# Kernel tuning notes

Hardware: AMD Instinct MI355X
Metric: run time of the kernel (lower is better)

The kernel has to match this reference:

```python
import jax, jax.numpy as jnp
import numpy as np
import math

BITS = 4
THRESH = 0.999
N_HEADS = 32
KV_HEADS = 8
HEAD_DIM = 128
ROPE_THETA = 10000.0


def _lower_median(x, axis):
    # torch.median returns the LOWER of the two middle values for even n
    n = x.shape[axis]
    xs = jnp.sort(x, axis=axis)
    return jnp.take(xs, jnp.array([(n - 1) // 2]), axis=axis)  # keepdims


def fake_quant_sparse(x, bits, axis, thresh):
    # simulated_quantize with include_sparse=True, dynamicquantization=True,
    # first_few_fp16=-1, clamp=False (faithful to KVQuant quant_fn_zp)
    x = x.astype(jnp.float32)
    t = 1.0 - (1.0 - thresh) / 2.0
    upper = jnp.quantile(x, t, axis=axis, keepdims=True)
    lower = jnp.quantile(x, 1.0 - t, axis=axis, keepdims=True)
    mask = (x <= lower) | (x >= upper)  # outlier mask
    med = _lower_median(x, axis)
    outliers = x * mask
    tmp = x - outliers + med * mask  # replace outliers with median
    maxval = jnp.max(tmp, axis=axis, keepdims=True)
    minval = jnp.min(tmp, axis=axis, keepdims=True)
    qx = (2 ** bits - 1) / (maxval - minval)
    offset = minval * qx  # clamp=False path
    inp = x - outliers
    q = jnp.clip(jnp.round(qx * inp - offset), 0.0, 2 ** bits - 1)
    deq = (q + offset) / qx
    out = jnp.where(mask, x, deq)  # qinp_out[mask]=0 then + outliers
    return jnp.nan_to_num(out, nan=0.0, posinf=0.0, neginf=0.0)


def _rotate_half(x):
    h = x.shape[-1] // 2
    return jnp.concatenate([-x[..., h:], x[..., :h]], axis=-1)


def _rope_cos_sin(position_ids, head_dim, theta):
    inv_freq = 1.0 / (theta ** (jnp.arange(0, head_dim, 2, dtype=jnp.float32) / head_dim))
    freqs = position_ids.astype(jnp.float32)[..., None] * inv_freq  # [B,S,hd/2]
    emb = jnp.concatenate([freqs, freqs], axis=-1)                   # [B,S,hd]
    return jnp.cos(emb), jnp.sin(emb)


def setup_inputs() -> dict:
    key = jax.random.key(0)
    ks = jax.random.split(key, 5)
    B, S, H = 2, 1024, 4096
    kv_dim = KV_HEADS * HEAD_DIM
    scale = 1.0 / math.sqrt(H)
    hidden_states = jax.random.normal(ks[0], (B, S, H), jnp.float32)
    Wq = jax.random.normal(ks[1], (H, H), jnp.float32) * scale
    Wk = jax.random.normal(ks[2], (kv_dim, H), jnp.float32) * scale
    Wv = jax.random.normal(ks[3], (kv_dim, H), jnp.float32) * scale
    Wo = jax.random.normal(ks[4], (H, H), jnp.float32) * scale
    position_ids = jnp.broadcast_to(jnp.arange(S, dtype=jnp.int32)[None, :], (B, S))
    attention_mask = jnp.broadcast_to(jnp.tril(jnp.ones((S, S), dtype=bool))[None, None], (B, 1, S, S))
    return {"hidden_states": hidden_states, "Wq": Wq, "Wk": Wk, "Wv": Wv,
            "Wo": Wo, "position_ids": position_ids, "attention_mask": attention_mask}


def reference(hidden_states, Wq, Wk, Wv, Wo, position_ids, attention_mask):
    B, S, H = hidden_states.shape
    groups = N_HEADS // KV_HEADS

    q = (hidden_states @ Wq.T).reshape(B, S, N_HEADS, HEAD_DIM).transpose(0, 2, 1, 3)
    k = hidden_states @ Wk.T  # [B,S,kv_dim]
    v = hidden_states @ Wv.T

    # Pre-RoPE quantization: K per-channel (axis 0 over B*S tokens), V per-token
    k_flat = fake_quant_sparse(k.reshape(B * S, -1), BITS, 0, THRESH)
    v_flat = fake_quant_sparse(v.reshape(B * S, -1), BITS, -1, THRESH)
    k = k_flat.reshape(B, S, KV_HEADS, HEAD_DIM).transpose(0, 2, 1, 3)
    v = v_flat.reshape(B, S, KV_HEADS, HEAD_DIM).transpose(0, 2, 1, 3)

    cos, sin = _rope_cos_sin(position_ids, HEAD_DIM, ROPE_THETA)
    cos, sin = cos[:, None], sin[:, None]  # [B,1,S,hd]
    q = q * cos + _rotate_half(q) * sin
    k = k * cos + _rotate_half(k) * sin

    k = jnp.repeat(k, groups, axis=1)  # repeat_kv -> [B,n_heads,S,hd]
    v = jnp.repeat(v, groups, axis=1)

    scores = jnp.einsum('bhqd,bhkd->bhqk', q, k) / math.sqrt(HEAD_DIM)
    scores = jnp.where(attention_mask, scores, jnp.finfo(jnp.float32).min)
    probs = jax.nn.softmax(scores.astype(jnp.float32), axis=-1).astype(q.dtype)
    attn = jnp.einsum('bhqk,bhkd->bhqd', probs, v)
    attn = attn.transpose(0, 2, 1, 3).reshape(B, S, -1)
    return attn @ Wo.T
```

## Files before the change

kernel.cpp:

```cpp
#include <hip/hip_runtime.h>

#define S_LEN 1024
#define B_SZ 2
#define H_DIM 4096
#define NHEADS 32
#define KVHEADS 8
#define HDIM 128
#define KV_DIM 1024
#define BS_C 2048

typedef _Float16 half8 __attribute__((ext_vector_type(8)));
typedef float f4 __attribute__((ext_vector_type(4)));
typedef unsigned short ushort_t;

static __device__ __forceinline__ ushort_t f2h(float x) {
  _Float16 h = (_Float16)x;
  return __builtin_bit_cast(unsigned short, h);
}
static __device__ __forceinline__ float h2f(ushort_t u) {
  return (float)__builtin_bit_cast(_Float16, u);
}

static __device__ __forceinline__ void gl2lds16(const void* g, void* l) {
  __builtin_amdgcn_global_load_lds(
      (const __attribute__((address_space(1))) unsigned int*)(unsigned long long)(uintptr_t)g,
      (__attribute__((address_space(3))) unsigned int*)(unsigned int)(uintptr_t)l,
      16, 0, 0);
}

__global__ __launch_bounds__(256) void cvt16(const float* __restrict__ x,
                                             ushort_t* __restrict__ h, int n4) {
  int i = blockIdx.x * 256 + threadIdx.x;
  if (i >= n4) return;
  float4 v = ((const float4*)x)[i];
  uint2 hp;
  hp.x = (unsigned)f2h(v.x) | ((unsigned)f2h(v.y) << 16);
  hp.y = (unsigned)f2h(v.z) | ((unsigned)f2h(v.w) << 16);
  ((uint2*)h)[i] = hp;
}

__global__ __launch_bounds__(256) void gemm_qkv(const ushort_t* __restrict__ Ahg,
                                                const ushort_t* __restrict__ Bhg,
                                                ushort_t* __restrict__ Qout,
                                                float* __restrict__ KVout) {
  __shared__ short Ah[128 * 32];
  __shared__ short Bh[128 * 32];
  const int K = 4096;
  const int tid = threadIdx.x;
  const int wid = tid >> 6;
  const int lane = tid & 63;
  const int ln = lane & 15;
  const int quad = lane >> 4;
  const int wx = wid & 1, wy = wid >> 1;
  const int m0 = blockIdx.y * 128, n0 = blockIdx.x * 128;
  const int sr = tid >> 2, sc = (tid & 3) * 8;

  const ushort_t* ap0 = Ahg + (size_t)(m0 + sr) * K + sc;
  const ushort_t* bp0 = Bhg + (size_t)(n0 + sr) * K + sc;
  const size_t rs = (size_t)64 * K;

  f4 acc[4][4];
#pragma unroll
  for (int i = 0; i < 4; i++)
#pragma unroll
    for (int j = 0; j < 4; j++) acc[i][j] = (f4){0.f, 0.f, 0.f, 0.f};

  for (int kk = 0; kk < K; kk += 32) {
    gl2lds16(ap0 + kk,      &Ah[tid * 8]);
    gl2lds16(ap0 + kk + rs, &Ah[2048 + tid * 8]);
    gl2lds16(bp0 + kk,      &Bh[tid * 8]);
    gl2lds16(bp0 + kk + rs, &Bh[2048 + tid * 8]);
    __syncthreads();

    half8 af[4], bfr[4];
#pragma unroll
    for (int mi = 0; mi < 4; mi++)
      af[mi] = *(const half8*)&Ah[(wy * 64 + mi * 16 + ln) * 32 + quad * 8];
#pragma unroll
    for (int ni = 0; ni < 4; ni++)
      bfr[ni] = *(const half8*)&Bh[(wx * 64 + ni * 16 + ln) * 32 + quad * 8];
    __syncthreads();

#pragma unroll
    for (int mi = 0; mi < 4; mi++)
#pragma unroll
      for (int ni = 0; ni < 4; ni++)
        acc[mi][ni] = __builtin_amdgcn_mfma_f32_16x16x32_f16(af[mi], bfr[ni], acc[mi][ni], 0, 0, 0);
  }

#pragma unroll
  for (int mi = 0; mi < 4; mi++) {
    int m = m0 + wy * 64 + mi * 16 + quad * 4;
#pragma unroll
    for (int ni = 0; ni < 4; ni++) {
      int n = n0 + wx * 64 + ni * 16 + ln;
      if (n0 < 4096) {
        ushort_t* cp = Qout + (size_t)m * 4096 + n;
#pragma unroll
        for (int r = 0; r < 4; r++) cp[(size_t)r * 4096] = f2h(acc[mi][ni][r]);
      } else {
        float* cp = KVout + (size_t)m * 2048 + (n - 4096);
#pragma unroll
        for (int r = 0; r < 4; r++) cp[(size_t)r * 2048] = acc[mi][ni][r];
      }
    }
  }
}

__global__ __launch_bounds__(256) void gemm_o(const ushort_t* __restrict__ Ahg,
                                              const ushort_t* __restrict__ Bhg,
                                              float* __restrict__ C0,
                                              float* __restrict__ C1) {
  __shared__ short Ah[128 * 32];
  __shared__ short Bh[128 * 32];
  const int K = 4096;
  const int tid = threadIdx.x;
  const int wid = tid >> 6;
  const int lane = tid & 63;
  const int ln = lane & 15;
  const int quad = lane >> 4;
  const int wx = wid & 1, wy = wid >> 1;
  const int m0 = blockIdx.y * 128, n0 = blockIdx.x * 128;
  const int kz = blockIdx.z * 2048;
  const int sr = tid >> 2, sc = (tid & 3) * 8;

  const ushort_t* ap0 = Ahg + (size_t)(m0 + sr) * K + kz + sc;
  const ushort_t* bp0 = Bhg + (size_t)(n0 + sr) * K + kz + sc;
  const size_t rs = (size_t)64 * K;

  f4 acc[4][4];
#pragma unroll
  for (int i = 0; i < 4; i++)
#pragma unroll
    for (int j = 0; j < 4; j++) acc[i][j] = (f4){0.f, 0.f, 0.f, 0.f};

  for (int kk = 0; kk < 2048; kk += 32) {
    gl2lds16(ap0 + kk,      &Ah[tid * 8]);
    gl2lds16(ap0 + kk + rs, &Ah[2048 + tid * 8]);
    gl2lds16(bp0 + kk,      &Bh[tid * 8]);
    gl2lds16(bp0 + kk + rs, &Bh[2048 + tid * 8]);
    __syncthreads();

    half8 af[4], bfr[4];
#pragma unroll
    for (int mi = 0; mi < 4; mi++)
      af[mi] = *(const half8*)&Ah[(wy * 64 + mi * 16 + ln) * 32 + quad * 8];
#pragma unroll
    for (int ni = 0; ni < 4; ni++)
      bfr[ni] = *(const half8*)&Bh[(wx * 64 + ni * 16 + ln) * 32 + quad * 8];
    __syncthreads();

#pragma unroll
    for (int mi = 0; mi < 4; mi++)
#pragma unroll
      for (int ni = 0; ni < 4; ni++)
        acc[mi][ni] = __builtin_amdgcn_mfma_f32_16x16x32_f16(af[mi], bfr[ni], acc[mi][ni], 0, 0, 0);
  }

  float* Cp = blockIdx.z ? C1 : C0;
#pragma unroll
  for (int mi = 0; mi < 4; mi++) {
    int m = m0 + wy * 64 + mi * 16 + quad * 4;
#pragma unroll
    for (int ni = 0; ni < 4; ni++) {
      int n = n0 + wx * 64 + ni * 16 + ln;
      float* cp = Cp + (size_t)m * 4096 + n;
#pragma unroll
      for (int r = 0; r < 4; r++) cp[(size_t)r * 4096] = acc[mi][ni][r];
    }
  }
}

__global__ __launch_bounds__(256) void reduce2(float* __restrict__ out,
                                               const float* __restrict__ p1, int n4) {
  int i = blockIdx.x * 256 + threadIdx.x;
  if (i >= n4) return;
  float4 a = ((const float4*)out)[i];
  float4 b = ((const float4*)p1)[i];
  a.x += b.x; a.y += b.y; a.z += b.z; a.w += b.w;
  ((float4*)out)[i] = a;
}

__global__ __launch_bounds__(256) void kquant(float* __restrict__ KV) {
  __shared__ float s[2048];
  __shared__ float red[256];
  const int c = blockIdx.x, tid = threadIdx.x;
  float x[8];
#pragma unroll
  for (int i = 0; i < 8; i++) {
    x[i] = KV[(size_t)(tid + i * 256) * 2048 + c];
    s[tid + i * 256] = x[i];
  }
  __syncthreads();
  for (int k = 2; k <= 2048; k <<= 1)
    for (int j = k >> 1; j > 0; j >>= 1) {
      for (int i = tid; i < 2048; i += 256) {
        int l = i ^ j;
        if (l > i) {
          float a = s[i], b2 = s[l];
          bool up = ((i & k) == 0);
          if ((a > b2) == up) { s[i] = b2; s[l] = a; }
        }
      }
      __syncthreads();
    }
  float lower = s[1]    + 0.0235f * (s[2]    - s[1]);
  float upper = s[2045] + 0.9765f * (s[2046] - s[2045]);
  float med   = s[1023];
  float mx = -__builtin_inff(), mn = __builtin_inff();
#pragma unroll
  for (int i = 0; i < 8; i++) {
    bool m = (x[i] <= lower) | (x[i] >= upper);
    float t = m ? med : x[i];
    mx = fmaxf(mx, t);
    mn = fminf(mn, t);
  }
  __syncthreads();
  red[tid] = mx; __syncthreads();
  for (int off = 128; off > 0; off >>= 1) {
    if (tid < off) red[tid] = fmaxf(red[tid], red[tid + off]);
    __syncthreads();
  }
  mx = red[0]; __syncthreads();
  red[tid] = mn; __syncthreads();
  for (int off = 128; off > 0; off >>= 1) {
    if (tid < off) red[tid] = fminf(red[tid], red[tid + off]);
    __syncthreads();
  }
  mn = red[0];
  float qx = 15.0f / (mx - mn);
  float offv = mn * qx;
#pragma unroll
  for (int i = 0; i < 8; i++) {
    bool m = (x[i] <= lower) | (x[i] >= upper);
    float inp = m ? 0.f : x[i];
    float q = rintf(qx * inp - offv);
    q = fminf(fmaxf(q, 0.f), 15.f);
    float deq = (q + offv) / qx;
    float o = m ? x[i] : deq;
    if (!__builtin_isfinite(o)) o = 0.f;
    KV[(size_t)(tid + i * 256) * 2048 + c] = o;
  }
}

__global__ __launch_bounds__(256) void vquant(const float* __restrict__ KV,
                                              ushort_t* __restrict__ vrow) {
  __shared__ float s[1024];
  __shared__ float red[256];
  const int rrow = blockIdx.x, tid = threadIdx.x;
  float x[4];
#pragma unroll
  for (int i = 0; i < 4; i++) {
    x[i] = KV[(size_t)rrow * 2048 + 1024 + tid + i * 256];
    s[tid + i * 256] = x[i];
  }
  __syncthreads();
  for (int k = 2; k <= 1024; k <<= 1)
    for (int j = k >> 1; j > 0; j >>= 1) {
      for (int i = tid; i < 1024; i += 256) {
        int l = i ^ j;
        if (l > i) {
          float a = s[i], b2 = s[l];
          bool up = ((i & k) == 0);
          if ((a > b2) == up) { s[i] = b2; s[l] = a; }
        }
      }
      __syncthreads();
    }
  float lower = s[0]    + 0.5115f * (s[1]    - s[0]);
  float upper = s[1022] + 0.4885f * (s[1023] - s[1022]);
  float med   = s[511];
  float mx = -__builtin_inff(), mn = __builtin_inff();
#pragma unroll
  for (int i = 0; i < 4; i++) {
    bool m = (x[i] <= lower) | (x[i] >= upper);
    float t = m ? med : x[i];
    mx = fmaxf(mx, t);
    mn = fminf(mn, t);
  }
  __syncthreads();
  red[tid] = mx; __syncthreads();
  for (int off = 128; off > 0; off >>= 1) {
    if (tid < off) red[tid] = fmaxf(red[tid], red[tid + off]);
    __syncthreads();
  }
  mx = red[0]; __syncthreads();
  red[tid] = mn; __syncthreads();
  for (int off = 128; off > 0; off >>= 1) {
    if (tid < off) red[tid] = fminf(red[tid], red[tid + off]);
    __syncthreads();
  }
  mn = red[0];
  float qx = 15.0f / (mx - mn);
  float offv = mn * qx;
#pragma unroll
  for (int i = 0; i < 4; i++) {
    bool m = (x[i] <= lower) | (x[i] >= upper);
    float inp = m ? 0.f : x[i];
    float q = rintf(qx * inp - offv);
    q = fminf(fmaxf(q, 0.f), 15.f);
    float deq = (q + offv) / qx;
    float o = m ? x[i] : deq;
    if (!__builtin_isfinite(o)) o = 0.f;
    vrow[(size_t)rrow * 1024 + tid + i * 256] = f2h(o);
  }
}

__global__ __launch_bounds__(256) void vtrans(const ushort_t* __restrict__ vrow,
                                              ushort_t* __restrict__ vb) {
  __shared__ ushort_t T[64 * 65];
  const int c0 = blockIdx.x * 64, r0 = blockIdx.y * 64;
  const int b = r0 >> 10, sbase = r0 & 1023;
#pragma unroll
  for (int i = 0; i < 2; i++) {
    int idx = threadIdx.x + i * 256;
    int r = idx >> 3, c8 = (idx & 7) * 8;
    uint4 v = *(const uint4*)(vrow + (size_t)(r0 + r) * 1024 + c0 + c8);
    const ushort_t* p = (const ushort_t*)&v;
#pragma unroll
    for (int j = 0; j < 8; j++) T[r * 65 + c8 + j] = p[j];
  }
  __syncthreads();
#pragma unroll
  for (int i = 0; i < 2; i++) {
    int idx = threadIdx.x + i * 256;
    int c = idx >> 3, s8 = (idx & 7) * 8;
    ushort_t tmp[8];
#pragma unroll
    for (int j = 0; j < 8; j++) tmp[j] = T[(s8 + j) * 65 + c];
    int gc = c0 + c;
    size_t oa = ((size_t)(b * KVHEADS + (gc >> 7)) * HDIM + (gc & 127)) * S_LEN + sbase + s8;
    *(uint4*)(vb + oa) = *(const uint4*)tmp;
  }
}

__global__ __launch_bounds__(256) void rope_q(const ushort_t* __restrict__ Q,
                                              const int* __restrict__ pos,
                                              ushort_t* __restrict__ qb) {
  int t = blockIdx.x * 256 + threadIdx.x;
  int i = t & 63;
  int h = (t >> 6) & 31;
  int s = (t >> 11) & 1023;
  int b = t >> 21;
  int p = pos[b * S_LEN + s];
  float inv = expf(-9.210340371976184f * ((float)i * (1.0f / 64.0f)));
  float ang = (float)p * inv;
  float sn, cs;
  sincosf(ang, &sn, &cs);
  size_t base = ((size_t)(b * S_LEN + s)) * H_DIM + h * HDIM + i;
  float x1 = h2f(Q[base]), x2 = h2f(Q[base + 64]);
  const float sc = 0.08838834764831845f;
  size_t ob = (((size_t)(b * NHEADS + h)) * S_LEN + s) * HDIM + i;
  qb[ob]      = f2h((x1 * cs - x2 * sn) * sc);
  qb[ob + 64] = f2h((x2 * cs + x1 * sn) * sc);
}

__global__ __launch_bounds__(256) void rope_k(const float* __restrict__ KV,
                                              const int* __restrict__ pos,
                                              ushort_t* __restrict__ kb) {
  int t = blockIdx.x * 256 + threadIdx.x;
  int i = t & 63;
  int h = (t >> 6) & 7;
  int s = (t >> 9) & 1023;
  int b = t >> 19;
  int p = pos[b * S_LEN + s];
  float inv = expf(-9.210340371976184f * ((float)i * (1.0f / 64.0f)));
  float ang = (float)p * inv;
  float sn, cs;
  sincosf(ang, &sn, &cs);
  size_t base = ((size_t)(b * S_LEN + s)) * 2048 + h * HDIM + i;
  float k1 = KV[base], k2 = KV[base + 64];
  size_t ob = (((size_t)(b * KVHEADS + h)) * S_LEN + s) * HDIM + i;
  kb[ob]      = f2h(k1 * cs - k2 * sn);
  kb[ob + 64] = f2h(k2 * cs + k1 * sn);
}

__global__ __launch_bounds__(256) void attn_fwd(const ushort_t* __restrict__ qb,
                                                const ushort_t* __restrict__ kb,
                                                const ushort_t* __restrict__ vb,
                                                ushort_t* __restrict__ ob) {
  __shared__ short Ks[64 * 136];
  __shared__ short Vs[128 * 72];
  __shared__ short Ps[4 * 32 * 72];
  const int tid = threadIdx.x;
  const int wid = tid >> 6;
  const int lane = tid & 63;
  const int ln = lane & 15;
  const int quad = lane >> 4;
  const int q0 = blockIdx.x * 128;
  const int bh = blockIdx.y;
  const int b = bh >> 5, h = bh & 31, hk = h >> 2;

  half8 aq[2][4];
#pragma unroll
  for (int mi = 0; mi < 2; mi++) {
    const ushort_t* qrow =
        qb + (((size_t)(b * NHEADS + h)) * S_LEN + q0 + wid * 32 + mi * 16 + ln) * HDIM;
#pragma unroll
    for (int ks = 0; ks < 4; ks++) aq[mi][ks] = *(const half8*)(qrow + ks * 32 + quad * 8);
  }

  f4 accO[2][8];
#pragma unroll
  for (int mi = 0; mi < 2; mi++)
#pragma unroll
    for (int i = 0; i < 8; i++) accO[mi][i] = (f4){0.f, 0.f, 0.f, 0.f};
  float mr[2][4], lr[2][4];
#pragma unroll
  for (int mi = 0; mi < 2; mi++)
#pragma unroll
    for (int r = 0; r < 4; r++) { mr[mi][r] = -__builtin_inff(); lr[mi][r] = 0.f; }

  const ushort_t* kbp = kb + ((size_t)(b * KVHEADS + hk)) * S_LEN * HDIM;
  const ushort_t* vbp = vb + ((size_t)(b * KVHEADS + hk)) * HDIM * S_LEN;

  const int ktiles = 2 * blockIdx.x + 2;
  for (int kt = 0; kt < ktiles; kt++) {
    const int k0 = kt * 64;
    __syncthreads();
#pragma unroll
    for (int cc = 0; cc < 4; cc++) {
      int idx = tid + cc * 256;
      int r = idx >> 4, c8 = idx & 15;
      *(uint4*)&Ks[r * 136 + c8 * 8] = *(const uint4*)(kbp + (size_t)(k0 + r) * HDIM + c8 * 8);
      int d = idx >> 3, s8 = idx & 7;
      *(uint4*)&Vs[d * 72 + s8 * 8] = *(const uint4*)(vbp + (size_t)d * S_LEN + k0 + s8 * 8);
    }
    __syncthreads();

    if (q0 + wid * 32 + 31 < k0) continue;

    f4 sc[2][4];
#pragma unroll
    for (int mi = 0; mi < 2; mi++)
#pragma unroll
      for (int nt = 0; nt < 4; nt++) sc[mi][nt] = (f4){0.f, 0.f, 0.f, 0.f};
#pragma unroll
    for (int nt = 0; nt < 4; nt++) {
      half8 bk[4];
#pragma unroll
      for (int ks = 0; ks < 4; ks++)
        bk[ks] = *(const half8*)&Ks[(nt * 16 + ln) * 136 + ks * 32 + quad * 8];
#pragma unroll
      for (int mi = 0; mi < 2; mi++)
#pragma unroll
        for (int ks = 0; ks < 4; ks++)
          sc[mi][nt] = __builtin_amdgcn_mfma_f32_16x16x32_f16(aq[mi][ks], bk[ks], sc[mi][nt], 0, 0, 0);
    }
#pragma unroll
    for (int mi = 0; mi < 2; mi++)
#pragma unroll
      for (int r = 0; r < 4; r++) {
        int mq = q0 + wid * 32 + mi * 16 + quad * 4 + r;
#pragma unroll
        for (int nt = 0; nt < 4; nt++) {
          int nk = k0 + nt * 16 + ln;
          if (nk > mq) sc[mi][nt][r] = -1e30f;
        }
      }
    float al[2][4];
#pragma unroll
    for (int mi = 0; mi < 2; mi++)
#pragma unroll
      for (int r = 0; r < 4; r++) {
        float tm = fmaxf(fmaxf(sc[mi][0][r], sc[mi][1][r]), fmaxf(sc[mi][2][r], sc[mi][3][r]));
        tm = fmaxf(tm, __shfl_xor(tm, 1));
        tm = fmaxf(tm, __shfl_xor(tm, 2));
        tm = fmaxf(tm, __shfl_xor(tm, 4));
        tm = fmaxf(tm, __shfl_xor(tm, 8));
        float mnew = fmaxf(mr[mi][r], tm);
        al[mi][r] = __expf(mr[mi][r] - mnew);
        mr[mi][r] = mnew;
        float ls = 0.f;
#pragma unroll
        for (int nt = 0; nt < 4; nt++) {
          float pp = __expf(sc[mi][nt][r] - mnew);
          sc[mi][nt][r] = pp;
          ls += pp;
        }
        ls += __shfl_xor(ls, 1);
        ls += __shfl_xor(ls, 2);
        ls += __shfl_xor(ls, 4);
        ls += __shfl_xor(ls, 8);
        lr[mi][r] = lr[mi][r] * al[mi][r] + ls;
      }
#pragma unroll
    for (int mi = 0; mi < 2; mi++)
#pragma unroll
      for (int dt = 0; dt < 8; dt++)
#pragma unroll
        for (int r = 0; r < 4; r++) accO[mi][dt][r] *= al[mi][r];
#pragma unroll
    for (int mi = 0; mi < 2; mi++)
#pragma unroll
      for (int r = 0; r < 4; r++)
#pragma unroll
        for (int nt = 0; nt < 4; nt++)
          Ps[wid * 2304 + (mi * 16 + quad * 4 + r) * 72 + nt * 16 + ln] =
              (short)f2h(sc[mi][nt][r]);
    half8 ap[2][2];
#pragma unroll
    for (int mi = 0; mi < 2; mi++)
#pragma unroll
      for (int k2 = 0; k2 < 2; k2++)
        ap[mi][k2] = *(const half8*)&Ps[wid * 2304 + (mi * 16 + ln) * 72 + k2 * 32 + quad * 8];
#pragma unroll
    for (int dt = 0; dt < 8; dt++)
#pragma unroll
      for (int k2 = 0; k2 < 2; k2++) {
        half8 bv = *(const half8*)&Vs[(dt * 16 + ln) * 72 + k2 * 32 + quad * 8];
#pragma unroll
        for (int mi = 0; mi < 2; mi++)
          accO[mi][dt] = __builtin_amdgcn_mfma_f32_16x16x32_f16(ap[mi][k2], bv, accO[mi][dt], 0, 0, 0);
      }
  }
#pragma unroll
  for (int mi = 0; mi < 2; mi++)
#pragma unroll
    for (int r = 0; r < 4; r++) {
      float invl = 1.0f / lr[mi][r];
      int so = q0 + wid * 32 + mi * 16 + quad * 4 + r;
      size_t obase = ((size_t)(b * S_LEN + so)) * H_DIM + h * HDIM;
#pragma unroll
      for (int dt = 0; dt < 8; dt++)
        ob[obase + dt * 16 + ln] = f2h(accO[mi][dt][r] * invl);
    }
}

extern "C" void kernel_launch(void* const* d_in, const int* in_sizes, int n_in,
                              void* d_out, int out_size, void* d_ws, size_t ws_size,
                              hipStream_t stream) {
  const float* hidden = (const float*)d_in[0];
  const float* Wq = (const float*)d_in[1];
  const float* Wk = (const float*)d_in[2];
  const float* Wv = (const float*)d_in[3];
  const float* Wo = (const float*)d_in[4];
  const int* pos = (const int*)d_in[5];
  float* outp = (float*)d_out;

  char* ws = (char*)d_ws;
  ushort_t* Wall = (ushort_t*)ws; ws += (size_t)6144 * 4096 * 2;
  ushort_t* hh   = (ushort_t*)ws; ws += (size_t)2048 * 4096 * 2;
  ushort_t* Qf16 = (ushort_t*)ws; ws += (size_t)2048 * 4096 * 2;
  float*    KVf  = (float*)ws;    ws += (size_t)2048 * 2048 * 4;
  ushort_t* vrow = (ushort_t*)ws; ws += (size_t)2048 * 1024 * 2;
  ushort_t* kb   = (ushort_t*)ws; ws += (size_t)2048 * 1024 * 2;
  ushort_t* vb   = (ushort_t*)ws;

  ushort_t* Woh = Wall;
  ushort_t* qb  = Wall + (size_t)4096 * 4096;
  ushort_t* ab  = hh;
  float*    P1  = (float*)Qf16;

  cvt16<<<8192, 256, 0, stream>>>(hidden, hh, 2048 * 4096 / 4);
  cvt16<<<16384, 256, 0, stream>>>(Wq, Wall, 4096 * 4096 / 4);
  cvt16<<<4096, 256, 0, stream>>>(Wk, Wall + (size_t)4096 * 4096, 1024 * 4096 / 4);
  cvt16<<<4096, 256, 0, stream>>>(Wv, Wall + (size_t)5120 * 4096, 1024 * 4096 / 4);

  gemm_qkv<<<dim3(48, 16), 256, 0, stream>>>(hh, Wall, Qf16, KVf);

  kquant<<<1024, 256, 0, stream>>>(KVf);
  vquant<<<2048, 256, 0, stream>>>(KVf, vrow);
  vtrans<<<dim3(16, 32), 256, 0, stream>>>(vrow, vb);

  rope_q<<<16384, 256, 0, stream>>>(Qf16, pos, qb);
  rope_k<<<4096, 256, 0, stream>>>(KVf, pos, kb);

  cvt16<<<16384, 256, 0, stream>>>(Wo, Woh, 4096 * 4096 / 4);

  attn_fwd<<<dim3(8, 64), 256, 0, stream>>>(qb, kb, vb, ab);

  gemm_o<<<dim3(32, 16, 2), 256, 0, stream>>>(ab, Woh, outp, P1);
  reduce2<<<8192, 256, 0, stream>>>(outp, P1, 2048 * 4096 / 4);
}
```

Baseline: 769.5 us.

## Rewrite GEMMs with 256x256 tiles, double-buffered LDS and swizzled layout

Both the QKV and output-projection GEMMs now share one core that computes 256x256 tiles with 512 threads. It double-buffers direct global-to-LDS loads with explicit vmcnt waits, so the next K-slice streams in while MFMAs run on the current one. The LDS layout is XOR-swizzled to avoid bank conflicts. Larger tiles raise operand reuse and cut global traffic, at the cost of fewer blocks (192 for QKV, 256 for O), which may underfill the CUs, and higher register and LDS use.

```diff
diff --git a/kernel.cpp b/kernel.cpp
--- a/kernel.cpp
+++ b/kernel.cpp
@@ -6,8 +6,6 @@
 #define NHEADS 32
 #define KVHEADS 8
 #define HDIM 128
-#define KV_DIM 1024
-#define BS_C 2048
 
 typedef _Float16 half8 __attribute__((ext_vector_type(8)));
 typedef float f4 __attribute__((ext_vector_type(4)));
@@ -27,6 +25,11 @@
       (__attribute__((address_space(3))) unsigned int*)(unsigned int)(uintptr_t)l,
       16, 0, 0);
 }
+
+#define WAITVM4 asm volatile("s_waitcnt vmcnt(4)" ::: "memory")
+#define WAITVM0 asm volatile("s_waitcnt vmcnt(0)" ::: "memory")
+#define BAR() __builtin_amdgcn_s_barrier()
+#define SCHED_FENCE() __builtin_amdgcn_sched_barrier(0)
 
 __global__ __launch_bounds__(256) void cvt16(const float* __restrict__ x,
                                              ushort_t* __restrict__ h, int n4) {
@@ -39,134 +42,140 @@
   ((uint2*)h)[i] = hp;
 }
 
-__global__ __launch_bounds__(256) void gemm_qkv(const ushort_t* __restrict__ Ahg,
-                                                const ushort_t* __restrict__ Bhg,
-                                                ushort_t* __restrict__ Qout,
-                                                float* __restrict__ KVout) {
-  __shared__ short Ah[128 * 32];
-  __shared__ short Bh[128 * 32];
-  const int K = 4096;
+
+static __device__ __forceinline__ void stage_tile(const ushort_t* __restrict__ src,
+                                                  char* ldsBase, int tid) {
+  const int r = tid >> 2;
+  const int c = ((tid & 3) ^ (r & 3)) << 3;
+  gl2lds16(src + (size_t)r * 4096 + c, ldsBase + tid * 16);
+  gl2lds16(src + (size_t)(r + 128) * 4096 + c, ldsBase + 8192 + tid * 16);
+}
+
+static __device__ __forceinline__ void gemm256_core(
+    const ushort_t* __restrict__ Ahg, const ushort_t* __restrict__ Bhg,
+    int m0, int n0, int kbase, int NT, char* lds, f4 (&acc)[8][4]) {
   const int tid = threadIdx.x;
   const int wid = tid >> 6;
   const int lane = tid & 63;
   const int ln = lane & 15;
   const int quad = lane >> 4;
-  const int wx = wid & 1, wy = wid >> 1;
-  const int m0 = blockIdx.y * 128, n0 = blockIdx.x * 128;
-  const int sr = tid >> 2, sc = (tid & 3) * 8;
-
-  const ushort_t* ap0 = Ahg + (size_t)(m0 + sr) * K + sc;
-  const ushort_t* bp0 = Bhg + (size_t)(n0 + sr) * K + sc;
-  const size_t rs = (size_t)64 * K;
-
-  f4 acc[4][4];
-#pragma unroll
-  for (int i = 0; i < 4; i++)
-#pragma unroll
-    for (int j = 0; j < 4; j++) acc[i][j] = (f4){0.f, 0.f, 0.f, 0.f};
-
-  for (int kk = 0; kk < K; kk += 32) {
-    gl2lds16(ap0 + kk,      &Ah[tid * 8]);
-    gl2lds16(ap0 + kk + rs, &Ah[2048 + tid * 8]);
-    gl2lds16(bp0 + kk,      &Bh[tid * 8]);
-    gl2lds16(bp0 + kk + rs, &Bh[2048 + tid * 8]);
-    __syncthreads();
-
-    half8 af[4], bfr[4];
-#pragma unroll
-    for (int mi = 0; mi < 4; mi++)
-      af[mi] = *(const half8*)&Ah[(wy * 64 + mi * 16 + ln) * 32 + quad * 8];
-#pragma unroll
-    for (int ni = 0; ni < 4; ni++)
-      bfr[ni] = *(const half8*)&Bh[(wx * 64 + ni * 16 + ln) * 32 + quad * 8];
-    __syncthreads();
-
-#pragma unroll
-    for (int mi = 0; mi < 4; mi++)
-#pragma unroll
-      for (int ni = 0; ni < 4; ni++)
-        acc[mi][ni] = __builtin_amdgcn_mfma_f32_16x16x32_f16(af[mi], bfr[ni], acc[mi][ni], 0, 0, 0);
-  }
-
-#pragma unroll
-  for (int mi = 0; mi < 4; mi++) {
-    int m = m0 + wy * 64 + mi * 16 + quad * 4;
-#pragma unroll
-    for (int ni = 0; ni < 4; ni++) {
-      int n = n0 + wx * 64 + ni * 16 + ln;
-      if (n0 < 4096) {
-        ushort_t* cp = Qout + (size_t)m * 4096 + n;
-#pragma unroll
-        for (int r = 0; r < 4; r++) cp[(size_t)r * 4096] = f2h(acc[mi][ni][r]);
-      } else {
-        float* cp = KVout + (size_t)m * 2048 + (n - 4096);
-#pragma unroll
-        for (int r = 0; r < 4; r++) cp[(size_t)r * 2048] = acc[mi][ni][r];
-      }
-    }
-  }
-}
-
-__global__ __launch_bounds__(256) void gemm_o(const ushort_t* __restrict__ Ahg,
-                                              const ushort_t* __restrict__ Bhg,
-                                              float* __restrict__ C0,
-                                              float* __restrict__ C1) {
-  __shared__ short Ah[128 * 32];
-  __shared__ short Bh[128 * 32];
-  const int K = 4096;
+  const int wy = wid >> 2, wx = wid & 3;
+  const int chunk = (quad ^ (ln & 3)) << 4;
+
+  const ushort_t* Abase = Ahg + (size_t)m0 * 4096 + kbase;
+  const ushort_t* Bbase = Bhg + (size_t)n0 * 4096 + kbase;
+
+  stage_tile(Abase, lds, tid);
+  stage_tile(Bbase, lds + 32768, tid);
+
+  int cur = 0;
+  for (int t = 0; t < NT; ++t) {
+    const bool st = (t + 1 < NT);
+    char* aCur = lds + cur * 16384;
+    char* bCur = lds + 32768 + cur * 16384;
+    if (st) {
+      stage_tile(Abase + (t + 1) * 32, lds + (cur ^ 1) * 16384, tid);
+      stage_tile(Bbase + (t + 1) * 32, lds + 32768 + (cur ^ 1) * 16384, tid);
+      WAITVM4;
+    } else {
+      WAITVM0;
+    }
+    BAR();
+    SCHED_FENCE();
+
+    half8 Af[8], Bf[4];
+#pragma unroll
+    for (int mi = 0; mi < 8; ++mi) {
+      int row = wy * 16 + mi * 32 + ln;
+      Af[mi] = *(const half8*)(aCur + row * 64 + chunk);
+    }
+#pragma unroll
+    for (int ni = 0; ni < 4; ++ni) {
+      int row = wx * 16 + ni * 64 + ln;
+      Bf[ni] = *(const half8*)(bCur + row * 64 + chunk);
+    }
+    __builtin_amdgcn_s_setprio(1);
+#pragma unroll
+    for (int mi = 0; mi < 8; ++mi)
+#pragma unroll
+      for (int ni = 0; ni < 4; ++ni)
+        acc[mi][ni] = __builtin_amdgcn_mfma_f32_16x16x32_f16(Af[mi], Bf[ni], acc[mi][ni], 0, 0, 0);
+    __builtin_amdgcn_s_setprio(0);
+    BAR();
+    cur ^= 1;
+  }
+}
+
+__global__ __launch_bounds__(512, 2) void gemm_qkv(const ushort_t* __restrict__ Ahg,
+                                                   const ushort_t* __restrict__ Bhg,
+                                                   ushort_t* __restrict__ Qout,
+                                                   float* __restrict__ KVout) {
+  __shared__ __align__(16) char lds[65536];
+  f4 acc[8][4];
+#pragma unroll
+  for (int i = 0; i < 8; ++i)
+#pragma unroll
+    for (int j = 0; j < 4; ++j) acc[i][j] = (f4){0.f, 0.f, 0.f, 0.f};
+  const int m0 = blockIdx.y * 256, n0 = blockIdx.x * 256;
+  gemm256_core(Ahg, Bhg, m0, n0, 0, 128, lds, acc);
+
   const int tid = threadIdx.x;
-  const int wid = tid >> 6;
-  const int lane = tid & 63;
-  const int ln = lane & 15;
-  const int quad = lane >> 4;
-  const int wx = wid & 1, wy = wid >> 1;
-  const int m0 = blockIdx.y * 128, n0 = blockIdx.x * 128;
+  const int wid = tid >> 6, lane = tid & 63, ln = lane & 15, quad = lane >> 4;
+  const int wy = wid >> 2, wx = wid & 3;
+  if (n0 < 4096) {
+#pragma unroll
+    for (int mi = 0; mi < 8; ++mi) {
+      int row = m0 + wy * 16 + mi * 32 + quad * 4;
+#pragma unroll
+      for (int ni = 0; ni < 4; ++ni) {
+        int col = n0 + wx * 16 + ni * 64 + ln;
+        ushort_t* cp = Qout + (size_t)row * 4096 + col;
+#pragma unroll
+        for (int r = 0; r < 4; ++r) cp[(size_t)r * 4096] = f2h(acc[mi][ni][r]);
+      }
+    }
+  } else {
+#pragma unroll
+    for (int mi = 0; mi < 8; ++mi) {
+      int row = m0 + wy * 16 + mi * 32 + quad * 4;
+#pragma unroll
+      for (int ni = 0; ni < 4; ++ni) {
+        int col = n0 - 4096 + wx * 16 + ni * 64 + ln;
+        float* cp = KVout + (size_t)row * 2048 + col;
+#pragma unroll
+        for (int r = 0; r < 4; ++r) cp[(size_t)r * 2048] = acc[mi][ni][r];
+      }
+    }
+  }
+}
+
+__global__ __launch_bounds__(512, 2) void gemm_o(const ushort_t* __restrict__ Ahg,
+                                                 const ushort_t* __restrict__ Bhg,
+                                                 float* __restrict__ C0,
+                                                 float* __restrict__ C1) {
+  __shared__ __align__(16) char lds[65536];
+  f4 acc[8][4];
+#pragma unroll
+  for (int i = 0; i < 8; ++i)
+#pragma unroll
+    for (int j = 0; j < 4; ++j) acc[i][j] = (f4){0.f, 0.f, 0.f, 0.f};
+  const int m0 = blockIdx.y * 256, n0 = blockIdx.x * 256;
   const int kz = blockIdx.z * 2048;
-  const int sr = tid >> 2, sc = (tid & 3) * 8;
-
-  const ushort_t* ap0 = Ahg + (size_t)(m0 + sr) * K + kz + sc;
-  const ushort_t* bp0 = Bhg + (size_t)(n0 + sr) * K + kz + sc;
-  const size_t rs = (size_t)64 * K;
-
-  f4 acc[4][4];
-#pragma unroll
-  for (int i = 0; i < 4; i++)
-#pragma unroll
-    for (int j = 0; j < 4; j++) acc[i][j] = (f4){0.f, 0.f, 0.f, 0.f};
-
-  for (int kk = 0; kk < 2048; kk += 32) {
-    gl2lds16(ap0 + kk,      &Ah[tid * 8]);
-    gl2lds16(ap0 + kk + rs, &Ah[2048 + tid * 8]);
-    gl2lds16(bp0 + kk,      &Bh[tid * 8]);
-    gl2lds16(bp0 + kk + rs, &Bh[2048 + tid * 8]);
-    __syncthreads();
-
-    half8 af[4], bfr[4];
-#pragma unroll
-    for (int mi = 0; mi < 4; mi++)
-      af[mi] = *(const half8*)&Ah[(wy * 64 + mi * 16 + ln) * 32 + quad * 8];
-#pragma unroll
-    for (int ni = 0; ni < 4; ni++)
-      bfr[ni] = *(const half8*)&Bh[(wx * 64 + ni * 16 + ln) * 32 + quad * 8];
-    __syncthreads();
-
-#pragma unroll
-    for (int mi = 0; mi < 4; mi++)
-#pragma unroll
-      for (int ni = 0; ni < 4; ni++)
-        acc[mi][ni] = __builtin_amdgcn_mfma_f32_16x16x32_f16(af[mi], bfr[ni], acc[mi][ni], 0, 0, 0);
-  }
-
+  gemm256_core(Ahg, Bhg, m0, n0, kz, 64, lds, acc);
+
+  const int tid = threadIdx.x;
+  const int wid = tid >> 6, lane = tid & 63, ln = lane & 15, quad = lane >> 4;
+  const int wy = wid >> 2, wx = wid & 3;
   float* Cp = blockIdx.z ? C1 : C0;
 #pragma unroll
-  for (int mi = 0; mi < 4; mi++) {
-    int m = m0 + wy * 64 + mi * 16 + quad * 4;
-#pragma unroll
-    for (int ni = 0; ni < 4; ni++) {
-      int n = n0 + wx * 64 + ni * 16 + ln;
-      float* cp = Cp + (size_t)m * 4096 + n;
-#pragma unroll
-      for (int r = 0; r < 4; r++) cp[(size_t)r * 4096] = acc[mi][ni][r];
+  for (int mi = 0; mi < 8; ++mi) {
+    int row = m0 + wy * 16 + mi * 32 + quad * 4;
+#pragma unroll
+    for (int ni = 0; ni < 4; ++ni) {
+      int col = n0 + wx * 16 + ni * 64 + ln;
+      float* cp = Cp + (size_t)row * 4096 + col;
+#pragma unroll
+      for (int r = 0; r < 4; ++r) cp[(size_t)r * 4096] = acc[mi][ni][r];
     }
   }
 }
@@ -557,7 +566,7 @@
   cvt16<<<4096, 256, 0, stream>>>(Wk, Wall + (size_t)4096 * 4096, 1024 * 4096 / 4);
   cvt16<<<4096, 256, 0, stream>>>(Wv, Wall + (size_t)5120 * 4096, 1024 * 4096 / 4);
 
-  gemm_qkv<<<dim3(48, 16), 256, 0, stream>>>(hh, Wall, Qf16, KVf);
+  gemm_qkv<<<dim3(24, 8), 512, 0, stream>>>(hh, Wall, Qf16, KVf);
 
   kquant<<<1024, 256, 0, stream>>>(KVf);
   vquant<<<2048, 256, 0, stream>>>(KVf, vrow);
@@ -570,6 +579,6 @@
 
   attn_fwd<<<dim3(8, 64), 256, 0, stream>>>(qb, kb, vb, ab);
 
-  gemm_o<<<dim3(32, 16, 2), 256, 0, stream>>>(ab, Woh, outp, P1);
+  gemm_o<<<dim3(16, 8, 2), 512, 0, stream>>>(ab, Woh, outp, P1);
   reduce2<<<8192, 256, 0, stream>>>(outp, P1, 2048 * 4096 / 4);
 }
```

Result: faster. 692.0 us (-10.1%).
